# Kernel tuning notes

Hardware: AMD Instinct MI355X
Metric: run time of the kernel (lower is better)

## Reference

```python
import jax, jax.numpy as jnp
import numpy as np

TEMP = 0.3
K_ANCHORS = 512
SK_ITERS = 4  # max_iter=4 in the original; tol early-exit omitted (fixed small iter count)
EPS = 1e-12   # F.normalize clamp_min eps


def setup_inputs() -> dict:
    key = jax.random.key(0)
    k1, k2 = jax.random.split(key)
    x = jax.random.normal(k1, (16, 256, 64, 64), dtype=jnp.float32)
    some_idx = jax.random.randint(k2, (K_ANCHORS,), 0, 64 * 64, dtype=jnp.int32)
    return {"x": x, "some_idx": some_idx}


def sinkhorn_knopp(A):
    # A: [M, k], strictly positive. Normalize by total mass, then alternate
    # L1 column / row normalization (p=1 normalize on positive entries == sum-divide).
    A = A / A.sum()
    def body(A, _):
        A = A / jnp.clip(A.sum(axis=0, keepdims=True), EPS)  # columns
        A = A / jnp.clip(A.sum(axis=1, keepdims=True), EPS)  # rows
        return A, None
    A, _ = jax.lax.scan(body, A, None, length=SK_ITERS)
    return A


def reference(x, some_idx):
    N, C, H, W = x.shape
    k = some_idx.shape[0]
    # L2-normalize over channel dim (F.normalize dim=1)
    l2_x = x / jnp.clip(jnp.linalg.norm(x, axis=1, keepdims=True), EPS)
    # gather k random spatial anchors -> [N, C, k]
    some_x = jnp.take(l2_x.reshape(N, C, H * W), some_idx, axis=-1)
    # cosine scores [N, k, H, W]
    scores = jnp.einsum('nchw,nck->nkhw', l2_x, some_x)
    # flatten to [N*H*W, k], exponentiate, Sinkhorn-Knopp
    A = jnp.exp(scores.transpose(0, 2, 3, 1).reshape(-1, k) / TEMP)
    A = sinkhorn_knopp(A)
    Kmat = A.reshape(N, H, W, k).transpose(0, 3, 1, 2)  # [N, k, H, W]
    # reconstruct from anchors
    return jnp.einsum('nkhw,nck->nchw', Kmat, some_x)
```

## Files before the change

kernel.cpp:

```cpp
#include <hip/hip_runtime.h>
#include <hip/hip_bf16.h>
#include <hip/hip_fp16.h>

#define N_B 16
#define C_DIM 256
#define HW 4096
#define M_TOT (N_B*HW)
#define K_A 512
#define TEMP_INV (1.0f/0.3f)
#define EPS_SK 1e-12f

typedef _Float16 f16x8 __attribute__((ext_vector_type(8)));
typedef _Float16 f16x4 __attribute__((ext_vector_type(4)));
typedef float f32x4 __attribute__((ext_vector_type(4)));

#define GLOBAL_AS __attribute__((address_space(1)))
#define LDS_AS __attribute__((address_space(3)))
__device__ __forceinline__ void gload_lds16(const void* g, void* l){
    __builtin_amdgcn_global_load_lds((GLOBAL_AS const void*)g, (LDS_AS void*)l, 16, 0, 0);
}

__global__ __launch_bounds__(256) void k_init(float* u, float* v){
    int i = blockIdx.x*256 + threadIdx.x;
    if (i < M_TOT) u[i] = 1.0f;
    if (i < K_A)   v[i] = 1.0f;
}

__global__ __launch_bounds__(256) void k_normtrans(const float* __restrict__ x,
                                                   _Float16* __restrict__ Lt){
    __shared__ float tl[64][257];
    __shared__ float red[4][64];
    __shared__ float invs[64];
    int n   = blockIdx.x >> 6;
    int hw0 = (blockIdx.x & 63) * 64;
    int tx4 = threadIdx.x & 15;
    int cy  = threadIdx.x >> 4;
    const float* px = x + ((size_t)(n*C_DIM + cy))*HW + hw0 + tx4*4;
    #pragma unroll
    for (int r = 0; r < 16; ++r){
        float4 xv = *(const float4*)(px + (size_t)(r*16)*HW);
        int c = cy + r*16;
        tl[tx4*4+0][c] = xv.x;
        tl[tx4*4+1][c] = xv.y;
        tl[tx4*4+2][c] = xv.z;
        tl[tx4*4+3][c] = xv.w;
    }
    __syncthreads();
    int tx = threadIdx.x & 63, ty = threadIdx.x >> 6;
    float ss = 0.f;
    #pragma unroll
    for (int cc = 0; cc < 64; ++cc){
        float tv = tl[tx][cc*4 + ty];
        ss += tv*tv;
    }
    red[ty][tx] = ss;
    __syncthreads();
    if (ty == 0){
        float s = red[0][tx]+red[1][tx]+red[2][tx]+red[3][tx];
        invs[tx] = 1.0f / fmaxf(sqrtf(s), 1e-12f);
    }
    __syncthreads();
    #pragma unroll
    for (int r = 0; r < 16; ++r){
        int hwl = ty + r*4;
        float inv = invs[hwl];
        float4 a = *(const float4*)&tl[hwl][tx*4];
        f16x4 h;
        h[0] = (_Float16)(a.x*inv); h[1] = (_Float16)(a.y*inv);
        h[2] = (_Float16)(a.z*inv); h[3] = (_Float16)(a.w*inv);
        *(f16x4*)&Lt[((size_t)(n*HW + hw0 + hwl))*C_DIM + tx*4] = h;
    }
}

__global__ __launch_bounds__(256) void k_gather(const _Float16* __restrict__ Lt,
                                                const int* __restrict__ sidx,
                                                _Float16* __restrict__ sxT){
    int n  = blockIdx.y;
    int jj = blockIdx.x*8 + (threadIdx.x >> 5);
    int c8 = (threadIdx.x & 31) * 8;
    int p  = sidx[jj];
    *(f16x8*)&sxT[((size_t)(n*K_A + jj))*C_DIM + c8] =
        *(const f16x8*)&Lt[((size_t)(n*HW + p))*C_DIM + c8];
}

__global__ __launch_bounds__(256) void k_gemm1(const _Float16* __restrict__ Lt,
                                               const _Float16* __restrict__ sxT,
                                               _Float16* __restrict__ A0,
                                               float* __restrict__ part){
    __shared__ _Float16 As[2*128*32];
    __shared__ _Float16 Bs[2*128*32];
    __shared__ float colred[4][128];
    const int nb = blockIdx.z;
    const int mbase = blockIdx.x * 128;
    const int jbase = blockIdx.y * 128;
    const int t = threadIdx.x;
    const int lane = t & 63, w = t >> 6;
    const int wm = (w >> 1)*64, wn = (w & 1)*64;
    const int l15 = lane & 15, lq = lane >> 4;

    f32x4 acc[4][4] = {};
    const _Float16* pa = Lt  + ((size_t)(nb*HW  + mbase))*C_DIM;
    const _Float16* pb = sxT + ((size_t)(nb*K_A + jbase))*C_DIM;

    const int r0 = t >> 2, ch = t & 3;
    const int r1 = r0 + 64;
    const int cs0 = (ch ^ ((r0 >> 1) & 3)) << 3;
    const int cs1 = (ch ^ ((r1 >> 1) & 3)) << 3;

#define STAGE1(buf, kt) { int k0 = (kt)*32; \
    gload_lds16(pa + (size_t)r0*C_DIM + k0 + cs0, &As[(buf)*4096 + t*8]); \
    gload_lds16(pa + (size_t)r1*C_DIM + k0 + cs1, &As[(buf)*4096 + (256+t)*8]); \
    gload_lds16(pb + (size_t)r0*C_DIM + k0 + cs0, &Bs[(buf)*4096 + t*8]); \
    gload_lds16(pb + (size_t)r1*C_DIM + k0 + cs1, &Bs[(buf)*4096 + (256+t)*8]); }

    STAGE1(0, 0);
    __syncthreads();
    int cur = 0;
    for (int kt = 0; kt < 8; ++kt){
        if (kt < 7) STAGE1(cur^1, kt+1);
        f16x8 af[4], bf[4];
        #pragma unroll
        for (int mi = 0; mi < 4; ++mi){
            int r = wm + mi*16 + l15;
            af[mi] = *(const f16x8*)&As[cur*4096 + r*32 + ((lq ^ ((r>>1)&3)) << 3)];
        }
        #pragma unroll
        for (int ni = 0; ni < 4; ++ni){
            int r = wn + ni*16 + l15;
            bf[ni] = *(const f16x8*)&Bs[cur*4096 + r*32 + ((lq ^ ((r>>1)&3)) << 3)];
        }
        #pragma unroll
        for (int mi = 0; mi < 4; ++mi)
            #pragma unroll
            for (int ni = 0; ni < 4; ++ni)
                acc[mi][ni] = __builtin_amdgcn_mfma_f32_16x16x32_f16(af[mi], bf[ni], acc[mi][ni], 0, 0, 0);
        __syncthreads();
        cur ^= 1;
    }
    float csum[4] = {0.f, 0.f, 0.f, 0.f};
    #pragma unroll
    for (int mi = 0; mi < 4; ++mi)
        #pragma unroll
        for (int ni = 0; ni < 4; ++ni)
            #pragma unroll
            for (int r = 0; r < 4; ++r){
                int hw = mbase + wm + mi*16 + lq*4 + r;
                int j  = jbase + wn + ni*16 + l15;
                float e = __expf(acc[mi][ni][r] * TEMP_INV);
                A0[((size_t)(nb*HW + hw))*K_A + j] = (_Float16)e;
                csum[ni] += e;
            }
    #pragma unroll
    for (int ni = 0; ni < 4; ++ni){
        float cv = csum[ni];
        cv += __shfl_xor(cv, 16);
        cv += __shfl_xor(cv, 32);
        if (lane < 16) colred[w][wn + ni*16 + l15] = cv;
    }
    __syncthreads();
    if (t < 128){
        int jj = t;
        float s = (jj < 64) ? (colred[0][jj] + colred[2][jj])
                            : (colred[1][jj] + colred[3][jj]);
        part[((size_t)(nb*32 + blockIdx.x))*K_A + jbase + jj] = s;
    }
}

__global__ __launch_bounds__(64) void k_colfinish(const float* __restrict__ part,
                                                  float* __restrict__ v, int nchunks){
    int j = blockIdx.x;
    int lane = threadIdx.x;
    float s = 0.f;
    for (int r = lane; r < nchunks; r += 64) s += part[(size_t)r*K_A + j];
    #pragma unroll
    for (int off = 32; off; off >>= 1) s += __shfl_xor(s, off);
    if (lane == 0){
        float vo = v[j];
        v[j] = 128.0f * vo / fmaxf(vo * s, EPS_SK);
    }
}

__global__ __launch_bounds__(256) void k_fused(const _Float16* __restrict__ A0,
                                               const float* __restrict__ v,
                                               float* __restrict__ u,
                                               float* __restrict__ part){
    __shared__ float red[4][512];
    int b = blockIdx.x;
    int tg = threadIdx.x >> 6, lane = threadIdx.x & 63;
    float vr[8];
    const float* pv = v + (lane << 3);
    #pragma unroll
    for (int e = 0; e < 8; ++e) vr[e] = pv[e];
    float acc[8] = {};
    for (int it = 0; it < 16; ++it){
        int i = (b << 6) + (it << 2) + tg;
        f16x8 a = *(const f16x8*)&A0[(size_t)i*K_A + (lane << 3)];
        float r = 0.f;
        #pragma unroll
        for (int e = 0; e < 8; ++e) r += (float)a[e] * vr[e];
        #pragma unroll
        for (int off = 32; off; off >>= 1) r += __shfl_xor(r, off);
        float uo = u[i];
        float un = uo / fmaxf(uo * r, EPS_SK);
        if (lane == 0) u[i] = un;
        #pragma unroll
        for (int e = 0; e < 8; ++e) acc[e] += (float)a[e] * un;
    }
    #pragma unroll
    for (int e = 0; e < 8; ++e) red[tg][(lane<<3)+e] = acc[e];
    __syncthreads();
    if (tg == 0){
        #pragma unroll
        for (int e = 0; e < 8; ++e){
            int j = (lane<<3)+e;
            part[((size_t)b)*K_A + j] = red[0][j]+red[1][j]+red[2][j]+red[3][j];
        }
    }
}

__global__ __launch_bounds__(256) void k_sxvT(const _Float16* __restrict__ sxT,
                                              const float* __restrict__ v,
                                              _Float16* __restrict__ SXv){
    __shared__ float tl[64][65];
    int n  = blockIdx.z;
    int j0 = blockIdx.x * 64;
    int c0 = blockIdx.y * 64;
    int tx = threadIdx.x & 63, ty = threadIdx.x >> 6;
    #pragma unroll
    for (int r = 0; r < 16; ++r){
        int jl = ty + r*4;
        tl[jl][tx] = (float)sxT[((size_t)(n*K_A + j0 + jl))*C_DIM + c0 + tx] * v[j0 + jl];
    }
    __syncthreads();
    #pragma unroll
    for (int r = 0; r < 16; ++r){
        int cl = ty + r*4;
        SXv[((size_t)(n*C_DIM + c0 + cl))*K_A + j0 + tx] = (_Float16)tl[tx][cl];
    }
}

__global__ __launch_bounds__(256) void k_gemm2(const _Float16* __restrict__ SXv,
                                               const _Float16* __restrict__ A0,
                                               const float* __restrict__ v,
                                               const float* __restrict__ u,
                                               float* __restrict__ out){
    __shared__ _Float16 As[2*128*32];
    __shared__ _Float16 Bs[2*128*32];
    __shared__ _Float16 vsh[512];
    const int nb = blockIdx.z;
    const int mbase = blockIdx.x * 128;
    const int nbase = blockIdx.y * 128;
    const int t = threadIdx.x;
    const int lane = t & 63, w = t >> 6;
    const int wm = (w >> 1)*64, wn = (w & 1)*64;
    const int l15 = lane & 15, lq = lane >> 4;

    vsh[t]       = (_Float16)v[t];
    vsh[t + 256] = (_Float16)v[t + 256];

    f32x4 acc[4][4] = {};
    f32x4 racc[4] = {};
    const _Float16* pa = SXv + ((size_t)(nb*C_DIM + mbase))*K_A;
    const _Float16* pb = A0  + ((size_t)(nb*HW   + nbase))*K_A;

    const int r0 = t >> 2, ch = t & 3;
    const int r1 = r0 + 64;
    const int cs0 = (ch ^ ((r0 >> 1) & 3)) << 3;
    const int cs1 = (ch ^ ((r1 >> 1) & 3)) << 3;

#define STAGE2(buf, kt) { int k0 = (kt)*32; \
    gload_lds16(pa + (size_t)r0*K_A + k0 + cs0, &As[(buf)*4096 + t*8]); \
    gload_lds16(pa + (size_t)r1*K_A + k0 + cs1, &As[(buf)*4096 + (256+t)*8]); \
    gload_lds16(pb + (size_t)r0*K_A + k0 + cs0, &Bs[(buf)*4096 + t*8]); \
    gload_lds16(pb + (size_t)r1*K_A + k0 + cs1, &Bs[(buf)*4096 + (256+t)*8]); }

    STAGE2(0, 0);
    __syncthreads();
    int cur = 0;
    for (int kt = 0; kt < 16; ++kt){
        if (kt < 15) STAGE2(cur^1, kt+1);
        f16x8 af[4], bf[4], vf;
        vf = *(const f16x8*)&vsh[kt*32 + lq*8];
        #pragma unroll
        for (int mi = 0; mi < 4; ++mi){
            int r = wm + mi*16 + l15;
            af[mi] = *(const f16x8*)&As[cur*4096 + r*32 + ((lq ^ ((r>>1)&3)) << 3)];
        }
        #pragma unroll
        for (int ni = 0; ni < 4; ++ni){
            int r = wn + ni*16 + l15;
            bf[ni] = *(const f16x8*)&Bs[cur*4096 + r*32 + ((lq ^ ((r>>1)&3)) << 3)];
        }
        #pragma unroll
        for (int mi = 0; mi < 4; ++mi)
            #pragma unroll
            for (int ni = 0; ni < 4; ++ni)
                acc[mi][ni] = __builtin_amdgcn_mfma_f32_16x16x32_f16(af[mi], bf[ni], acc[mi][ni], 0, 0, 0);
        #pragma unroll
        for (int ni = 0; ni < 4; ++ni)
            racc[ni] = __builtin_amdgcn_mfma_f32_16x16x32_f16(vf, bf[ni], racc[ni], 0, 0, 0);
        __syncthreads();
        cur ^= 1;
    }
    float un[4];
    #pragma unroll
    for (int ni = 0; ni < 4; ++ni){
        float rv = racc[ni][0];
        float uo = u[nb*HW + nbase + wn + ni*16 + l15];
        un[ni] = uo / fmaxf(uo * rv, EPS_SK);
    }
    #pragma unroll
    for (int mi = 0; mi < 4; ++mi)
        #pragma unroll
        for (int ni = 0; ni < 4; ++ni)
            #pragma unroll
            for (int r = 0; r < 4; ++r){
                int c  = mbase + wm + mi*16 + lq*4 + r;
                int hw = nbase + wn + ni*16 + l15;
                out[((size_t)(nb*C_DIM + c))*HW + hw] = acc[mi][ni][r] * un[ni];
            }
}

extern "C" void kernel_launch(void* const* d_in, const int* in_sizes, int n_in,
                              void* d_out, int out_size, void* d_ws, size_t ws_size,
                              hipStream_t stream){
    const float* x  = (const float*)d_in[0];
    const int* sidx = (const int*)d_in[1];
    float* out = (float*)d_out;

    char* ws = (char*)d_ws;
    _Float16* Lt  = (_Float16*)ws;  ws += (size_t)N_B*HW*C_DIM*2;
    _Float16* A0  = (_Float16*)ws;  ws += (size_t)M_TOT*K_A*2;
    _Float16* sxT = (_Float16*)ws;  ws += (size_t)N_B*K_A*C_DIM*2;
    _Float16* SXv = (_Float16*)ws;  ws += (size_t)N_B*C_DIM*K_A*2;
    float*    u   = (float*)ws;     ws += (size_t)M_TOT*4;
    float*    v   = (float*)ws;     ws += (size_t)K_A*4;
    float*    part= (float*)ws;     ws += (size_t)1024*K_A*4;

    k_init     <<<256, 256, 0, stream>>>(u, v);
    k_normtrans<<<1024, 256, 0, stream>>>(x, Lt);
    k_gather   <<<dim3(64,16), 256, 0, stream>>>(Lt, sidx, sxT);
    k_gemm1    <<<dim3(32,4,16), 256, 0, stream>>>(Lt, sxT, A0, part);

    k_colfinish<<<512, 64, 0, stream>>>(part, v, 512);
    for (int it = 0; it < 3; ++it){
        k_fused    <<<1024, 256, 0, stream>>>(A0, v, u, part);
        k_colfinish<<<512, 64, 0, stream>>>(part, v, 1024);
    }

    k_sxvT <<<dim3(8,4,16), 256, 0, stream>>>(sxT, v, SXv);
    k_gemm2<<<dim3(2,32,16), 256, 0, stream>>>(SXv, A0, v, u, out);
}
```

Baseline: 174.6 us.

## Triple-buffer GEMM loads with explicit vmcnt waits, swizzle block order, fold init

Both GEMM kernels move from a double-buffered to a triple-buffered LDS pipeline. Explicit s_waitcnt vmcnt counts and raw barriers let two tiles stay in flight while MFMAs run on the third. Block indices are remapped from a 1D grid with an XCD-style swizzle, so neighbouring tiles share L2 on the same die. The u/v initialisation kernel is folded into k_normtrans to save a launch. The extra LDS per block may reduce occupancy, and the hand-written wait counts depend on each stage issuing exactly four loads per thread.

```diff
diff --git a/kernel.cpp b/kernel.cpp
--- a/kernel.cpp
+++ b/kernel.cpp
@@ -20,19 +20,17 @@
     __builtin_amdgcn_global_load_lds((GLOBAL_AS const void*)g, (LDS_AS void*)l, 16, 0, 0);
 }
 
-__global__ __launch_bounds__(256) void k_init(float* u, float* v){
-    int i = blockIdx.x*256 + threadIdx.x;
-    if (i < M_TOT) u[i] = 1.0f;
-    if (i < K_A)   v[i] = 1.0f;
-}
-
 __global__ __launch_bounds__(256) void k_normtrans(const float* __restrict__ x,
-                                                   _Float16* __restrict__ Lt){
+                                                   _Float16* __restrict__ Lt,
+                                                   float* __restrict__ u,
+                                                   float* __restrict__ v){
     __shared__ float tl[64][257];
     __shared__ float red[4][64];
     __shared__ float invs[64];
     int n   = blockIdx.x >> 6;
     int hw0 = (blockIdx.x & 63) * 64;
+    if (threadIdx.x < 64) u[blockIdx.x*64 + threadIdx.x] = 1.0f;
+    if (blockIdx.x < 2)   v[blockIdx.x*256 + threadIdx.x] = 1.0f;
     int tx4 = threadIdx.x & 15;
     int cy  = threadIdx.x >> 4;
     const float* px = x + ((size_t)(n*C_DIM + cy))*HW + hw0 + tx4*4;
@@ -87,12 +85,13 @@
                                                const _Float16* __restrict__ sxT,
                                                _Float16* __restrict__ A0,
                                                float* __restrict__ part){
-    __shared__ _Float16 As[2*128*32];
-    __shared__ _Float16 Bs[2*128*32];
+    __shared__ _Float16 As[3*128*32];
+    __shared__ _Float16 Bs[3*128*32];
     __shared__ float colred[4][128];
-    const int nb = blockIdx.z;
-    const int mbase = blockIdx.x * 128;
-    const int jbase = blockIdx.y * 128;
+    const int swz = (blockIdx.x & 7)*256 + (blockIdx.x >> 3);
+    const int jb = swz & 3, mb = (swz >> 2) & 31, nb = swz >> 7;
+    const int mbase = mb * 128;
+    const int jbase = jb * 128;
     const int t = threadIdx.x;
     const int lane = t & 63, w = t >> 6;
     const int wm = (w >> 1)*64, wn = (w & 1)*64;
@@ -113,11 +112,15 @@
     gload_lds16(pb + (size_t)r0*C_DIM + k0 + cs0, &Bs[(buf)*4096 + t*8]); \
     gload_lds16(pb + (size_t)r1*C_DIM + k0 + cs1, &Bs[(buf)*4096 + (256+t)*8]); }
 
-    STAGE1(0, 0);
-    __syncthreads();
-    int cur = 0;
+    STAGE1(0, 0); STAGE1(1, 1); STAGE1(2, 2);
+    #pragma unroll
     for (int kt = 0; kt < 8; ++kt){
-        if (kt < 7) STAGE1(cur^1, kt+1);
+        if (kt < 6)      asm volatile("s_waitcnt vmcnt(8)" ::: "memory");
+        else if (kt < 7) asm volatile("s_waitcnt vmcnt(4)" ::: "memory");
+        else             asm volatile("s_waitcnt vmcnt(0)" ::: "memory");
+        __builtin_amdgcn_s_barrier();
+        __builtin_amdgcn_sched_barrier(0);
+        const int cur = kt % 3;
         f16x8 af[4], bf[4];
         #pragma unroll
         for (int mi = 0; mi < 4; ++mi){
@@ -134,8 +137,9 @@
             #pragma unroll
             for (int ni = 0; ni < 4; ++ni)
                 acc[mi][ni] = __builtin_amdgcn_mfma_f32_16x16x32_f16(af[mi], bf[ni], acc[mi][ni], 0, 0, 0);
-        __syncthreads();
-        cur ^= 1;
+        __builtin_amdgcn_s_barrier();
+        __builtin_amdgcn_sched_barrier(0);
+        if (kt < 5) STAGE1((kt+3)%3, kt+3);
     }
     float csum[4] = {0.f, 0.f, 0.f, 0.f};
     #pragma unroll
@@ -162,7 +166,7 @@
         int jj = t;
         float s = (jj < 64) ? (colred[0][jj] + colred[2][jj])
                             : (colred[1][jj] + colred[3][jj]);
-        part[((size_t)(nb*32 + blockIdx.x))*K_A + jbase + jj] = s;
+        part[((size_t)(nb*32 + mb))*K_A + jbase + jj] = s;
     }
 }
 
@@ -244,12 +248,13 @@
                                                const float* __restrict__ v,
                                                const float* __restrict__ u,
                                                float* __restrict__ out){
-    __shared__ _Float16 As[2*128*32];
-    __shared__ _Float16 Bs[2*128*32];
+    __shared__ _Float16 As[3*128*32];
+    __shared__ _Float16 Bs[3*128*32];
     __shared__ _Float16 vsh[512];
-    const int nb = blockIdx.z;
-    const int mbase = blockIdx.x * 128;
-    const int nbase = blockIdx.y * 128;
+    const int swz = (blockIdx.x & 7)*128 + (blockIdx.x >> 3);
+    const int mb = swz & 1, nbi = (swz >> 1) & 31, nb = swz >> 6;
+    const int mbase = mb * 128;
+    const int nbase = nbi * 128;
     const int t = threadIdx.x;
     const int lane = t & 63, w = t >> 6;
     const int wm = (w >> 1)*64, wn = (w & 1)*64;
@@ -274,11 +279,15 @@
     gload_lds16(pb + (size_t)r0*K_A + k0 + cs0, &Bs[(buf)*4096 + t*8]); \
     gload_lds16(pb + (size_t)r1*K_A + k0 + cs1, &Bs[(buf)*4096 + (256+t)*8]); }
 
-    STAGE2(0, 0);
-    __syncthreads();
-    int cur = 0;
+    STAGE2(0, 0); STAGE2(1, 1); STAGE2(2, 2);
+    #pragma unroll
     for (int kt = 0; kt < 16; ++kt){
-        if (kt < 15) STAGE2(cur^1, kt+1);
+        if (kt < 14)      asm volatile("s_waitcnt vmcnt(8)" ::: "memory");
+        else if (kt < 15) asm volatile("s_waitcnt vmcnt(4)" ::: "memory");
+        else              asm volatile("s_waitcnt vmcnt(0)" ::: "memory");
+        __builtin_amdgcn_s_barrier();
+        __builtin_amdgcn_sched_barrier(0);
+        const int cur = kt % 3;
         f16x8 af[4], bf[4], vf;
         vf = *(const f16x8*)&vsh[kt*32 + lq*8];
         #pragma unroll
@@ -299,8 +308,9 @@
         #pragma unroll
         for (int ni = 0; ni < 4; ++ni)
             racc[ni] = __builtin_amdgcn_mfma_f32_16x16x32_f16(vf, bf[ni], racc[ni], 0, 0, 0);
-        __syncthreads();
-        cur ^= 1;
+        __builtin_amdgcn_s_barrier();
+        __builtin_amdgcn_sched_barrier(0);
+        if (kt < 13) STAGE2((kt+3)%3, kt+3);
     }
     float un[4];
     #pragma unroll
@@ -337,10 +347,9 @@
     float*    v   = (float*)ws;     ws += (size_t)K_A*4;
     float*    part= (float*)ws;     ws += (size_t)1024*K_A*4;
 
-    k_init     <<<256, 256, 0, stream>>>(u, v);
-    k_normtrans<<<1024, 256, 0, stream>>>(x, Lt);
+    k_normtrans<<<1024, 256, 0, stream>>>(x, Lt, u, v);
     k_gather   <<<dim3(64,16), 256, 0, stream>>>(Lt, sidx, sxT);
-    k_gemm1    <<<dim3(32,4,16), 256, 0, stream>>>(Lt, sxT, A0, part);
+    k_gemm1    <<<2048, 256, 0, stream>>>(Lt, sxT, A0, part);
 
     k_colfinish<<<512, 64, 0, stream>>>(part, v, 512);
     for (int it = 0; it < 3; ++it){
@@ -349,5 +358,5 @@
     }
 
     k_sxvT <<<dim3(8,4,16), 256, 0, stream>>>(sxT, v, SXv);
-    k_gemm2<<<dim3(2,32,16), 256, 0, stream>>>(SXv, A0, v, u, out);
-}
+    k_gemm2<<<1024, 256, 0, stream>>>(SXv, A0, v, u, out);
+}
```

Result: faster. 157.4 us (median of 2 runs) (-9.8%).
